# Kernel optimization log

Measured on AMD Instinct MI355X. Metric: run time of the kernel, lower is better.

The kernel has to match this reference:

```python
import jax, jax.numpy as jnp
import numpy as np
from jax import lax

K = 3          # kernel_size
STRIDE = 1
PAD = 1
DIL = 1


def conv2d(x, w, b):
    y = lax.conv_general_dilated(
        x, w, (STRIDE, STRIDE), [(PAD, PAD), (PAD, PAD)],
        rhs_dilation=(DIL, DIL),
        dimension_numbers=('NCHW', 'OIHW', 'NCHW'))
    return y + b[None, :, None, None]


def setup_inputs() -> dict:
    key = jax.random.key(0)
    ks = jax.random.split(key, 6)
    N, Cin, Cout, H, W = 4, 64, 64, 192, 192
    K2 = K * K
    x_input = jax.random.normal(ks[0], (N, Cin, H, W), jnp.float32)
    # offset branch: 2*K2 output channels (dy, dx per kernel tap); small init
    w_off = jax.random.normal(ks[1], (2 * K2, Cin, K, K), jnp.float32) * 0.01
    b_off = jnp.zeros((2 * K2,), jnp.float32)
    # modulation branch (DCNv2): K2 channels, 2*sigmoid
    w_mod = jax.random.normal(ks[2], (K2, Cin, K, K), jnp.float32) * 0.01
    b_mod = jnp.zeros((K2,), jnp.float32)
    # main conv weight + bias
    w = jax.random.normal(ks[3], (Cout, Cin, K, K), jnp.float32) / np.sqrt(Cin * K2)
    b = jax.random.normal(ks[4], (Cout,), jnp.float32) * 0.01
    return {'x_input': x_input, 'w_off': w_off, 'b_off': b_off,
            'w_mod': w_mod, 'b_mod': b_mod, 'w': w, 'b': b}


def _deform_sample(x, py, px):
    # x [N,C,H,W]; py,px [N,K2,Ho,Wo] -> bilinear samples [N,C,K2,Ho,Wo]
    N, C, H, W = x.shape
    xf = x.reshape(N, C, H * W)
    y0 = jnp.floor(py)
    x0 = jnp.floor(px)
    ly = py - y0
    lx = px - x0
    y0i = y0.astype(jnp.int32)
    x0i = x0.astype(jnp.int32)

    def gather(yi, xi, wt):
        valid = (yi >= 0) & (yi < H) & (xi >= 0) & (xi < W)  # zero padding outside
        idx = jnp.clip(yi, 0, H - 1) * W + jnp.clip(xi, 0, W - 1)
        idx_flat = idx.reshape(N, -1)
        vals = jax.vmap(lambda a, i: jnp.take(a, i, axis=1))(xf, idx_flat)  # [N,C,K2*Ho*Wo]
        vals = vals.reshape(N, C, *yi.shape[1:])
        return vals * (wt * valid)[:, None]

    out = gather(y0i, x0i, (1 - ly) * (1 - lx))
    out = out + gather(y0i, x0i + 1, (1 - ly) * lx)
    out = out + gather(y0i + 1, x0i, ly * (1 - lx))
    out = out + gather(y0i + 1, x0i + 1, ly * lx)
    return out


def reference(x_input, w_off, b_off, w_mod, b_mod, w, b):
    N, C, H, W = x_input.shape
    K2 = K * K
    off = conv2d(x_input, w_off, b_off)                       # [N,2*K2,Ho,Wo]
    mod = 2.0 * jax.nn.sigmoid(conv2d(x_input, w_mod, b_mod))  # [N,K2,Ho,Wo]
    Ho, Wo = off.shape[2], off.shape[3]
    off = off.reshape(N, K2, 2, Ho, Wo)
    ky = jnp.repeat(jnp.arange(K) * DIL, K).astype(jnp.float32)  # [K2]
    kx = jnp.tile(jnp.arange(K) * DIL, K).astype(jnp.float32)
    hy = (jnp.arange(Ho) * STRIDE - PAD).astype(jnp.float32)
    wx = (jnp.arange(Wo) * STRIDE - PAD).astype(jnp.float32)
    py = off[:, :, 0] + hy[None, None, :, None] + ky[None, :, None, None]  # [N,K2,Ho,Wo]
    px = off[:, :, 1] + wx[None, None, None, :] + kx[None, :, None, None]
    val = _deform_sample(x_input, py, px) * mod[:, None]       # [N,C,K2,Ho,Wo]
    out = jnp.einsum('nckhw,ock->nohw', val, w.reshape(w.shape[0], C, K2))
    out = out + b[None, :, None, None]
    return jax.nn.relu(out)
```

## Files before the change

### kernel.cpp

```cpp
#include <hip/hip_runtime.h>
#include <hip/hip_bf16.h>
#include <hip/hip_fp16.h>
#include <math.h>


#define NB   4
#define CIN  64
#define COUT 64
#define HH   192
#define WW   192
#define HW   (HH*WW)

typedef __attribute__((ext_vector_type(4))) float f32x4;
typedef __attribute__((ext_vector_type(8))) _Float16 f16x8;
typedef __attribute__((ext_vector_type(4))) unsigned int u32x4;

__device__ __forceinline__ int iclamp(int v, int lo, int hi) {
    return v < lo ? lo : (v > hi ? hi : v);
}
__device__ __forceinline__ unsigned short f16bits(float f) {
    __half h = __float2half(f);
    union { __half h; unsigned short u; } t; t.h = h; return t.u;
}
__device__ __forceinline__ float h2f(unsigned short u) {
    union { unsigned short u; __half h; } t; t.u = u; return __half2float(t.h);
}
__device__ __forceinline__ __half2 dup_lo(unsigned int u) {
    unsigned int lo = u & 0xffffu;
    unsigned int d = lo | (lo << 16);
    union { unsigned int u; __half2 h; } t; t.u = d; return t.h;
}
__device__ __forceinline__ __half2 dup_hi(unsigned int u) {
    unsigned int hi = u >> 16;
    unsigned int d = hi | (hi << 16);
    union { unsigned int u; __half2 h; } t; t.u = d; return t.h;
}

__global__ __launch_bounds__(256) void to_nhwc(
        const float* __restrict__ x, unsigned short* __restrict__ xt) {
    int n  = blockIdx.y;
    int px = blockIdx.x * 256 + threadIdx.x;
    const float* xn = x + (size_t)n * CIN * HW + px;
    union { unsigned short us[64]; u32x4 q[8]; } pk;
#pragma unroll
    for (int c = 0; c < 64; c++) pk.us[c] = f16bits(xn[c * HW]);
    u32x4* dst = (u32x4*)(xt + ((size_t)n * HW + px) * 64);
#pragma unroll
    for (int i = 0; i < 8; i++) dst[i] = pk.q[i];
}

__global__ __launch_bounds__(256) void prep_weights(
        const float* __restrict__ w, const float* __restrict__ w_off,
        const float* __restrict__ w_mod, const float* __restrict__ b_off,
        const float* __restrict__ b_mod, unsigned short* __restrict__ wfrag,
        unsigned short* __restrict__ wauxf, float* __restrict__ baux) {
    int idx = blockIdx.x * 256 + threadIdx.x;
    if (idx < 36864) {
        int j    = idx & 7;
        int lane = (idx >> 3) & 63;
        int kc   = (idx >> 9) & 1;
        int g    = (idx >> 10) & 3;
        int k    = idx >> 12;
        int o = g * 16 + (lane & 15);
        int c = kc * 32 + (lane >> 4) * 8 + j;
        wfrag[idx] = f16bits(w[(o * 64 + c) * 9 + k]);
    }
    if (idx < 18432) {
        int j    = idx & 7;
        int lane = (idx >> 3) & 63;
        int kc   = (idx >> 9) & 1;
        int ga   = (idx >> 10) & 1;
        int k    = idx >> 11;
        int o = ga * 16 + (lane & 15);
        int c = kc * 32 + (lane >> 4) * 8 + j;
        float v = 0.f;
        if (o < 18)      v = w_off[(o * 64 + c) * 9 + k];
        else if (o < 27) v = w_mod[((o - 18) * 64 + c) * 9 + k];
        wauxf[idx] = f16bits(v);
    }
    if (idx < 32) {
        float v = 0.f;
        if (idx < 18)      v = b_off[idx];
        else if (idx < 27) v = b_mod[idx - 18];
        baux[idx] = v;
    }
}

__global__ __launch_bounds__(256, 4) void dcn_fused(
        const unsigned short* __restrict__ xt,
        const unsigned short* __restrict__ wfrag,
        const unsigned short* __restrict__ wauxf,
        const float* __restrict__ baux,
        const float* __restrict__ bias,
        float* __restrict__ out) {
    __shared__ __align__(16) unsigned short win[216 * 64];
    __shared__ __align__(16) unsigned short oml[2][32][32];
    __shared__ __align__(16) u32x4 plan[576];

    int tid = threadIdx.x;
    int l   = tid & 63;
    int wv  = __builtin_amdgcn_readfirstlane(tid >> 6);
    int r2  = wv >> 1;
    int g2  = wv & 1;

    int id = blockIdx.x;
    int sw = (id & 7) * 288 + (id >> 3);
    int n  = sw / 576;
    int r  = sw % 576;
    int ho2    = (r / 6) * 2;
    int wobase = (r % 6) * 32;

    const char* xb = (const char*)xt + (size_t)n * HW * 128;

    if (tid < 216) {
        int rw = tid / 36, cl = tid - rw * 36;
        int gy = iclamp(ho2 - 2 + rw, 0, HH - 1);
        int gx = iclamp(wobase - 2 + cl, 0, WW - 1);
        const u32x4* src = (const u32x4*)(xb + ((size_t)gy * WW + gx) * 128);
        char* dst = (char*)win + tid * 128;
        int xw = (tid & 7) << 4;
#pragma unroll
        for (int c = 0; c < 8; c++)
            *(u32x4*)(dst + ((c * 16) ^ xw)) = src[c];
    }
    __syncthreads();

    {
        f32x4 aacc[2];
        aacc[0] = (f32x4){0.f, 0.f, 0.f, 0.f};
        aacc[1] = (f32x4){0.f, 0.f, 0.f, 0.f};
        const f16x8 zero8 = (f16x8){0, 0, 0, 0, 0, 0, 0, 0};
        int pa   = g2 * 16 + (l & 15);
        int cba  = (l >> 4) * 16;
        int ho_a = ho2 + r2;

#pragma unroll 1
        for (int k = 0; k < 9; k++) {
            int ky = k / 3, kx = k - 3 * (k / 3);
            int ys = ho_a + ky - 1;
            if ((unsigned)ys >= (unsigned)HH) continue;
            int xs = wobase + pa + kx - 1;
            bool ok = (unsigned)xs < (unsigned)WW;
            int sA = (ky + 1 + r2) * 36 + (pa + kx + 1);
            const char* pp = (const char*)win + sA * 128;
            int xw = (sA & 7) << 4;
            const f16x8* wa = ((const f16x8*)wauxf) + (k * 4) * 64 + l;
#pragma unroll
            for (int kc = 0; kc < 2; kc++) {
                f16x8 bv = *(const f16x8*)(pp + ((kc * 64 + cba) ^ xw));
                if (!ok) bv = zero8;
                f16x8 a0 = wa[(kc)     * 64];
                f16x8 a1 = wa[(2 + kc) * 64];
                aacc[0] = __builtin_amdgcn_mfma_f32_16x16x32_f16(a0, bv, aacc[0], 0, 0, 0);
                aacc[1] = __builtin_amdgcn_mfma_f32_16x16x32_f16(a1, bv, aacc[1], 0, 0, 0);
            }
        }
#pragma unroll
        for (int h = 0; h < 2; h++) {
#pragma unroll
            for (int rr = 0; rr < 2; rr++) {
                int o = h * 16 + (l >> 4) * 4 + rr * 2;
                float v0 = aacc[h][rr * 2]     + baux[o];
                float v1 = aacc[h][rr * 2 + 1] + baux[o + 1];
                if (o     >= 18) v0 = 2.f / (1.f + expf(-v0));
                if (o + 1 >= 18) v1 = 2.f / (1.f + expf(-v1));
                unsigned int pk = (unsigned int)f16bits(v0)
                                | ((unsigned int)f16bits(v1) << 16);
                *(unsigned int*)&oml[r2][pa][o] = pk;
            }
        }
    }
    __syncthreads();

    for (int i = tid; i < 576; i += 256) {
        int rp = i / 9;
        int k  = i - rp * 9;
        int r2p = rp >> 5, px = rp & 31;
        int ho_p  = ho2 + r2p;
        int wox_p = wobase + px;

        int ky = k / 3, kx = k - 3 * (k / 3);
        unsigned int oyx = *(const unsigned int*)&oml[r2p][px][2 * k];
        float offy = h2f((unsigned short)(oyx & 0xffffu));
        float offx = h2f((unsigned short)(oyx >> 16));
        float mm   = h2f(oml[r2p][px][18 + k]);
        float py  = offy + (float)(ho_p - 1 + ky);
        float pxf = offx + (float)(wox_p - 1 + kx);
        float y0f = floorf(py), x0f = floorf(pxf);
        float ly = py - y0f, lx = pxf - x0f;
        int y0 = (int)y0f, x0 = (int)x0f;
        int y1 = y0 + 1, x1 = x0 + 1;
        bool y0ok = (unsigned)y0 < (unsigned)HH, y1ok = (unsigned)y1 < (unsigned)HH;
        bool x0ok = (unsigned)x0 < (unsigned)WW, x1ok = (unsigned)x1 < (unsigned)WW;
        float wt0 = (y0ok && x0ok) ? mm * (1.f - ly) * (1.f - lx) : 0.f;
        float wt1 = (y0ok && x1ok) ? mm * (1.f - ly) * lx         : 0.f;
        float wt2 = (y1ok && x0ok) ? mm * ly * (1.f - lx)         : 0.f;
        float wt3 = (y1ok && x1ok) ? mm * ly * lx                 : 0.f;
        int y0c = iclamp(y0, 0, HH - 1), y1c = iclamp(y1, 0, HH - 1);
        int x0c = iclamp(x0, 0, WW - 1), x1c = iclamp(x1, 0, WW - 1);
        int sy0 = y0c - ho2 + 2,    sy1 = y1c - ho2 + 2;
        int sx0 = x0c - wobase + 2, sx1 = x1c - wobase + 2;
        int sy0c = iclamp(sy0, 0, 5),  sy1c = iclamp(sy1, 0, 5);
        int sx0c = iclamp(sx0, 0, 35), sx1c = iclamp(sx1, 0, 35);
        bool fb0 = (wt0 > 0.f) && ((sy0 != sy0c) | (sx0 != sx0c));
        bool fb1 = (wt1 > 0.f) && ((sy0 != sy0c) | (sx1 != sx1c));
        bool fb2 = (wt2 > 0.f) && ((sy1 != sy1c) | (sx0 != sx0c));
        bool fb3 = (wt3 > 0.f) && ((sy1 != sy1c) | (sx1 != sx1c));
        unsigned int c0 = fb0 ? 0xffffu : (unsigned int)(sy0c * 36 + sx0c);
        unsigned int c1 = fb1 ? 0xffffu : (unsigned int)(sy0c * 36 + sx1c);
        unsigned int c2 = fb2 ? 0xffffu : (unsigned int)(sy1c * 36 + sx0c);
        unsigned int c3 = fb3 ? 0xffffu : (unsigned int)(sy1c * 36 + sx1c);

        unsigned int w01 = (unsigned int)f16bits(wt0) | ((unsigned int)f16bits(wt1) << 16);
        unsigned int w23 = (unsigned int)f16bits(wt2) | ((unsigned int)f16bits(wt3) << 16);
        plan[i] = (u32x4){w01, w23, c0 | (c1 << 16), c2 | (c3 << 16)};
    }
    __syncthreads();

    f32x4 acc[4];
#pragma unroll
    for (int nf = 0; nf < 4; nf++) acc[nf] = (f32x4){0.f, 0.f, 0.f, 0.f};

    int p_loc = l & 15;
    int chunk = l >> 4;
    int p     = g2 * 16 + p_loc;
    int ho_w  = ho2 + r2;
    int wox   = wobase + p;
    int cb0   = chunk * 16;
    int cb1   = cb0 + 64;
    const u32x4* plp = plan + (r2 * 32 + p) * 9;
    const unsigned short* omp = &oml[r2][p][0];

    union Q { u32x4 u; __half2 h2[4]; };

#pragma unroll 1
    for (int k = 0; k < 9; k++) {
        const f16x8* wfk = ((const f16x8*)wfrag) + (k * 8) * 64 + l;
        f16x8 wB[8];
#pragma unroll
        for (int f = 0; f < 8; f++) wB[f] = wfk[f * 64];

        u32x4 pl = plp[k];
        unsigned int c0 = pl.z & 0xffffu, c1 = pl.z >> 16;
        unsigned int c2 = pl.w & 0xffffu, c3 = pl.w >> 16;

        int d0 = (int)(c0 & 255u), d1 = (int)(c1 & 255u);
        int d2 = (int)(c2 & 255u), d3 = (int)(c3 & 255u);
        const char* b0 = (const char*)win + d0 * 128;
        const char* b1 = (const char*)win + d1 * 128;
        const char* b2 = (const char*)win + d2 * 128;
        const char* b3 = (const char*)win + d3 * 128;
        int x0 = (d0 & 7) << 4, x1 = (d1 & 7) << 4;
        int x2 = (d2 & 7) << 4, x3 = (d3 & 7) << 4;
        Q q0, q1, q2, q3, q4, q5, q6, q7;
        q0.u = *(const u32x4*)(b0 + (cb0 ^ x0));
        q1.u = *(const u32x4*)(b0 + (cb1 ^ x0));
        q2.u = *(const u32x4*)(b1 + (cb0 ^ x1));
        q3.u = *(const u32x4*)(b1 + (cb1 ^ x1));
        q4.u = *(const u32x4*)(b2 + (cb0 ^ x2));
        q5.u = *(const u32x4*)(b2 + (cb1 ^ x2));
        q6.u = *(const u32x4*)(b3 + (cb0 ^ x3));
        q7.u = *(const u32x4*)(b3 + (cb1 ^ x3));

        if (__builtin_expect((c0 == 0xffffu) | (c1 == 0xffffu) |
                             (c2 == 0xffffu) | (c3 == 0xffffu), 0)) {
            int ky = k / 3, kx = k - 3 * (k / 3);
            unsigned int oyx = *(const unsigned int*)(omp + 2 * k);
            float offy = h2f((unsigned short)(oyx & 0xffffu));
            float offx = h2f((unsigned short)(oyx >> 16));
            float py  = offy + (float)(ho_w - 1 + ky);
            float pxf = offx + (float)(wox - 1 + kx);
            int y0 = (int)floorf(py), x0i = (int)floorf(pxf);
            int y0c = iclamp(y0, 0, HH - 1),     y1c = iclamp(y0 + 1, 0, HH - 1);
            int x0c = iclamp(x0i, 0, WW - 1),    x1c = iclamp(x0i + 1, 0, WW - 1);
            if (c0 == 0xffffu) { const char* gp = xb + ((size_t)y0c * WW + x0c) * 128 + cb0;
                                 q0.u = *(const u32x4*)gp; q1.u = *(const u32x4*)(gp + 64); }
            if (c1 == 0xffffu) { const char* gp = xb + ((size_t)y0c * WW + x1c) * 128 + cb0;
                                 q2.u = *(const u32x4*)gp; q3.u = *(const u32x4*)(gp + 64); }
            if (c2 == 0xffffu) { const char* gp = xb + ((size_t)y1c * WW + x0c) * 128 + cb0;
                                 q4.u = *(const u32x4*)gp; q5.u = *(const u32x4*)(gp + 64); }
            if (c3 == 0xffffu) { const char* gp = xb + ((size_t)y1c * WW + x1c) * 128 + cb0;
                                 q6.u = *(const u32x4*)gp; q7.u = *(const u32x4*)(gp + 64); }
        }

        __half2 wv0 = dup_lo(pl.x), wv1 = dup_hi(pl.x);
        __half2 wv2 = dup_lo(pl.y), wv3 = dup_hi(pl.y);
        union { __half2 h2[4]; f16x8 v; } fA0, fA1;
#pragma unroll
        for (int j = 0; j < 4; j++) {
            __half2 t = __hmul2(q0.h2[j], wv0);
            t = __hfma2(q2.h2[j], wv1, t);
            t = __hfma2(q4.h2[j], wv2, t);
            t = __hfma2(q6.h2[j], wv3, t);
            fA0.h2[j] = t;
            __half2 s = __hmul2(q1.h2[j], wv0);
            s = __hfma2(q3.h2[j], wv1, s);
            s = __hfma2(q5.h2[j], wv2, s);
            s = __hfma2(q7.h2[j], wv3, s);
            fA1.h2[j] = s;
        }

        __builtin_amdgcn_s_setprio(1);
#pragma unroll
        for (int nf = 0; nf < 4; nf++) {
            acc[nf] = __builtin_amdgcn_mfma_f32_16x16x32_f16(fA0.v, wB[nf * 2],     acc[nf], 0, 0, 0);
            acc[nf] = __builtin_amdgcn_mfma_f32_16x16x32_f16(fA1.v, wB[nf * 2 + 1], acc[nf], 0, 0, 0);
        }
        __builtin_amdgcn_s_setprio(0);
    }

#pragma unroll
    for (int nf = 0; nf < 4; nf++) {
        int o = nf * 16 + p_loc;
        float bo = bias[o];
        int wo = wobase + g2 * 16 + chunk * 4;
        float* op = out + (((size_t)n * COUT + o) * HH + ho_w) * WW + wo;
#pragma unroll
        for (int rr = 0; rr < 4; rr++) {
            float v = acc[nf][rr] + bo;
            op[rr] = fmaxf(v, 0.f);
        }
    }
}

extern "C" void kernel_launch(void* const* d_in, const int* in_sizes, int n_in,
                              void* d_out, int out_size, void* d_ws, size_t ws_size,
                              hipStream_t stream) {
    const float* x     = (const float*)d_in[0];
    const float* w_off = (const float*)d_in[1];
    const float* b_off = (const float*)d_in[2];
    const float* w_mod = (const float*)d_in[3];
    const float* b_mod = (const float*)d_in[4];
    const float* w     = (const float*)d_in[5];
    const float* b     = (const float*)d_in[6];
    float* out = (float*)d_out;

    unsigned short* wfrag = (unsigned short*)d_ws;
    unsigned short* wauxf = wfrag + 36864;
    float* baux = (float*)(wauxf + 18432);
    unsigned short* xt = (unsigned short*)(baux + 32);

    to_nhwc<<<dim3(144, NB), dim3(256), 0, stream>>>(x, xt);
    prep_weights<<<dim3(144), dim3(256), 0, stream>>>(w, w_off, w_mod, b_off,
                                                      b_mod, wfrag, wauxf, baux);
    dcn_fused<<<dim3(2304), dim3(256), 0, stream>>>(xt, wfrag, wauxf, baux, b, out);
}
```

Baseline: 71.47 us.

## Fuse NCHW-to-NHWC fp16 conversion into the DCN kernel's tile load

Removes the separate to_nhwc pre-pass and its fp16 NHWC scratch buffer. The fused kernel now reads fp32 NCHW input directly, converting to fp16 while staging the halo window into LDS, and converts on the fly in the rare out-of-window bilinear gather path. This saves one kernel launch plus a full write and re-read of the activation tensor. In exchange, each thread makes strided per-channel fp32 loads instead of contiguous 16-byte vector loads, and overlapping windows re-read halo pixels in fp32.

```diff
diff --git a/kernel.cpp b/kernel.cpp
--- a/kernel.cpp
+++ b/kernel.cpp
@@ -34,19 +34,6 @@
     unsigned int hi = u >> 16;
     unsigned int d = hi | (hi << 16);
     union { unsigned int u; __half2 h; } t; t.u = d; return t.h;
-}
-
-__global__ __launch_bounds__(256) void to_nhwc(
-        const float* __restrict__ x, unsigned short* __restrict__ xt) {
-    int n  = blockIdx.y;
-    int px = blockIdx.x * 256 + threadIdx.x;
-    const float* xn = x + (size_t)n * CIN * HW + px;
-    union { unsigned short us[64]; u32x4 q[8]; } pk;
-#pragma unroll
-    for (int c = 0; c < 64; c++) pk.us[c] = f16bits(xn[c * HW]);
-    u32x4* dst = (u32x4*)(xt + ((size_t)n * HW + px) * 64);
-#pragma unroll
-    for (int i = 0; i < 8; i++) dst[i] = pk.q[i];
 }
 
 __global__ __launch_bounds__(256) void prep_weights(
@@ -87,7 +74,7 @@
 }
 
 __global__ __launch_bounds__(256, 4) void dcn_fused(
-        const unsigned short* __restrict__ xt,
+        const float* __restrict__ x,
         const unsigned short* __restrict__ wfrag,
         const unsigned short* __restrict__ wauxf,
         const float* __restrict__ baux,
@@ -110,18 +97,23 @@
     int ho2    = (r / 6) * 2;
     int wobase = (r % 6) * 32;
 
-    const char* xb = (const char*)xt + (size_t)n * HW * 128;
+    const float* xn = x + (size_t)n * CIN * HW;
 
     if (tid < 216) {
         int rw = tid / 36, cl = tid - rw * 36;
         int gy = iclamp(ho2 - 2 + rw, 0, HH - 1);
         int gx = iclamp(wobase - 2 + cl, 0, WW - 1);
-        const u32x4* src = (const u32x4*)(xb + ((size_t)gy * WW + gx) * 128);
+        const float* xp = xn + gy * WW + gx;
         char* dst = (char*)win + tid * 128;
         int xw = (tid & 7) << 4;
 #pragma unroll
-        for (int c = 0; c < 8; c++)
-            *(u32x4*)(dst + ((c * 16) ^ xw)) = src[c];
+        for (int c8 = 0; c8 < 8; c8++) {
+            union { unsigned short us[8]; u32x4 q; } pk8;
+#pragma unroll
+            for (int j = 0; j < 8; j++)
+                pk8.us[j] = f16bits(xp[(c8 * 8 + j) * HW]);
+            *(u32x4*)(dst + ((c8 * 16) ^ xw)) = pk8.q;
+        }
     }
     __syncthreads();
 
@@ -228,10 +220,11 @@
     int wox   = wobase + p;
     int cb0   = chunk * 16;
     int cb1   = cb0 + 64;
+    int chb   = chunk * 8;
     const u32x4* plp = plan + (r2 * 32 + p) * 9;
     const unsigned short* omp = &oml[r2][p][0];
 
-    union Q { u32x4 u; __half2 h2[4]; };
+    union Q { u32x4 u; __half2 h2[4]; unsigned short us[8]; };
 
 #pragma unroll 1
     for (int k = 0; k < 9; k++) {
@@ -271,16 +264,40 @@
             float py  = offy + (float)(ho_w - 1 + ky);
             float pxf = offx + (float)(wox - 1 + kx);
             int y0 = (int)floorf(py), x0i = (int)floorf(pxf);
-            int y0c = iclamp(y0, 0, HH - 1),     y1c = iclamp(y0 + 1, 0, HH - 1);
-            int x0c = iclamp(x0i, 0, WW - 1),    x1c = iclamp(x0i + 1, 0, WW - 1);
-            if (c0 == 0xffffu) { const char* gp = xb + ((size_t)y0c * WW + x0c) * 128 + cb0;
-                                 q0.u = *(const u32x4*)gp; q1.u = *(const u32x4*)(gp + 64); }
-            if (c1 == 0xffffu) { const char* gp = xb + ((size_t)y0c * WW + x1c) * 128 + cb0;
-                                 q2.u = *(const u32x4*)gp; q3.u = *(const u32x4*)(gp + 64); }
-            if (c2 == 0xffffu) { const char* gp = xb + ((size_t)y1c * WW + x0c) * 128 + cb0;
-                                 q4.u = *(const u32x4*)gp; q5.u = *(const u32x4*)(gp + 64); }
-            if (c3 == 0xffffu) { const char* gp = xb + ((size_t)y1c * WW + x1c) * 128 + cb0;
-                                 q6.u = *(const u32x4*)gp; q7.u = *(const u32x4*)(gp + 64); }
+            int y0c = iclamp(y0, 0, HH - 1),  y1c = iclamp(y0 + 1, 0, HH - 1);
+            int x0c = iclamp(x0i, 0, WW - 1), x1c = iclamp(x0i + 1, 0, WW - 1);
+            if (c0 == 0xffffu) {
+                const float* gp = xn + y0c * WW + x0c;
+#pragma unroll
+                for (int j = 0; j < 8; j++) {
+                    q0.us[j] = f16bits(gp[(chb + j) * HW]);
+                    q1.us[j] = f16bits(gp[(chb + 32 + j) * HW]);
+                }
+            }
+            if (c1 == 0xffffu) {
+                const float* gp = xn + y0c * WW + x1c;
+#pragma unroll
+                for (int j = 0; j < 8; j++) {
+                    q2.us[j] = f16bits(gp[(chb + j) * HW]);
+                    q3.us[j] = f16bits(gp[(chb + 32 + j) * HW]);
+                }
+            }
+            if (c2 == 0xffffu) {
+                const float* gp = xn + y1c * WW + x0c;
+#pragma unroll
+                for (int j = 0; j < 8; j++) {
+                    q4.us[j] = f16bits(gp[(chb + j) * HW]);
+                    q5.us[j] = f16bits(gp[(chb + 32 + j) * HW]);
+                }
+            }
+            if (c3 == 0xffffu) {
+                const float* gp = xn + y1c * WW + x1c;
+#pragma unroll
+                for (int j = 0; j < 8; j++) {
+                    q6.us[j] = f16bits(gp[(chb + j) * HW]);
+                    q7.us[j] = f16bits(gp[(chb + 32 + j) * HW]);
+                }
+            }
         }
 
         __half2 wv0 = dup_lo(pl.x), wv1 = dup_hi(pl.x);
@@ -338,10 +355,8 @@
     unsigned short* wfrag = (unsigned short*)d_ws;
     unsigned short* wauxf = wfrag + 36864;
     float* baux = (float*)(wauxf + 18432);
-    unsigned short* xt = (unsigned short*)(baux + 32);
-
-    to_nhwc<<<dim3(144, NB), dim3(256), 0, stream>>>(x, xt);
+
     prep_weights<<<dim3(144), dim3(256), 0, stream>>>(w, w_off, w_mod, b_off,
                                                       b_mod, wfrag, wauxf, baux);
-    dcn_fused<<<dim3(2304), dim3(256), 0, stream>>>(xt, wfrag, wauxf, baux, b, out);
-}
+    dcn_fused<<<dim3(2304), dim3(256), 0, stream>>>(x, wfrag, wauxf, baux, b, out);
+}
```

Result: faster. 62.56 us, median of 3 (-12.5%).
